# Kernel optimization log

Hardware: AMD Instinct MI355X
Metric: run time of the kernel (lower is better)

Reference implementation:

```python
import jax, jax.numpy as jnp
import numpy as np

NH = 4        # n_head
L_TOPK = 16   # AWG top-k l
DEC = 2       # dec_layers
EPS = 1e-6


def _ln(x, g, b):
    m = jnp.mean(x, -1, keepdims=True)
    v = jnp.mean((x - m) ** 2, -1, keepdims=True)
    return (x - m) * jax.lax.rsqrt(v + EPS) * g + b


def _heads(x, W):
    B, L, C = x.shape
    return (x @ W).reshape(B, L, NH, C // NH).transpose(0, 2, 1, 3)  # [B,H,L,dk]


def _softmax_attn(qh, kh):
    dk = qh.shape[-1]
    logits = jnp.einsum('bhqd,bhkd->bhqk', qh / jnp.sqrt(jnp.float32(dk)), kh)
    return jax.nn.softmax(logits, axis=-1)


def cross_attn_block(q, k, v, Wq, Wk, Wv, Wo, g, b):
    B, Lq, C = q.shape
    a = _softmax_attn(_heads(q, Wq), _heads(k, Wk))
    o = jnp.einsum('bhqk,bhkd->bhqd', a, _heads(v, Wv))
    o = o.transpose(0, 2, 1, 3).reshape(B, Lq, C) @ Wo
    return _ln(o + q, g, b)


def awg_attn_block(q, k, v, Wq, Wk, Wv, Wo, g, b):
    # top-k attention-weight-gating: keep weights >= l-th largest, renormalize
    B, Lq, C = q.shape
    a = _softmax_attn(_heads(q, Wq), _heads(k, Wk))
    thr = jax.lax.top_k(a, L_TOPK)[0][..., -1:]          # [B,H,Lq,1]
    w = a * (a >= thr).astype(a.dtype)
    w = w / jnp.sum(w, -1, keepdims=True)
    o = jnp.einsum('bhqk,bhkd->bhqd', w, _heads(v, Wv))
    o = o.transpose(0, 2, 1, 3).reshape(B, Lq, C) @ Wo
    return _ln(o + q, g, b)


def setup_inputs() -> dict:
    key = jax.random.key(0)
    ks = jax.random.split(key, 32)
    B, Lq, Lk, C, F = 4, 3000, 750, 64, 256
    s = 1.0 / np.sqrt(C)
    sf = 1.0 / np.sqrt(F)
    d = {}
    d['q'] = jax.random.normal(ks[0], (B, Lq, C), jnp.float32)
    d['enc'] = jax.random.normal(ks[1], (B, Lk, C), jnp.float32)
    # cross_attn_layer params
    for i, n in enumerate(['cal_Wq', 'cal_Wk', 'cal_Wv', 'cal_Wo']):
        d[n] = jax.random.normal(ks[2 + i], (C, C), jnp.float32) * s
    d['cal_ln1_g'] = jnp.ones((C,), jnp.float32)
    d['cal_ln1_b'] = jnp.zeros((C,), jnp.float32)
    d['cal_W1'] = jax.random.normal(ks[6], (C, F), jnp.float32) * s
    d['cal_b1'] = jnp.zeros((F,), jnp.float32)
    d['cal_W2'] = jax.random.normal(ks[7], (F, C), jnp.float32) * sf
    d['cal_b2'] = jnp.zeros((C,), jnp.float32)
    d['cal_ln2_g'] = jnp.ones((C,), jnp.float32)
    d['cal_ln2_b'] = jnp.zeros((C,), jnp.float32)
    # stacked MGAN params [DEC, ...]
    d['m_ln_g'] = jnp.ones((DEC, C), jnp.float32)
    d['m_ln_b'] = jnp.zeros((DEC, C), jnp.float32)
    d['m_fc1_W'] = jax.random.normal(ks[8], (DEC, C, C), jnp.float32) * s
    d['m_fc1_b'] = jnp.zeros((DEC, C), jnp.float32)
    d['m_fc2_W'] = jax.random.normal(ks[9], (DEC, C, C), jnp.float32) * s
    d['m_fc2_b'] = jnp.zeros((DEC, C), jnp.float32)
    for i, n in enumerate(['m_Wq', 'm_Wk', 'm_Wv', 'm_Wo']):
        d[n] = jax.random.normal(ks[10 + i], (DEC, C, C), jnp.float32) * s
    d['m_aln_g'] = jnp.ones((DEC, C), jnp.float32)
    d['m_aln_b'] = jnp.zeros((DEC, C), jnp.float32)
    d['fc_W'] = jax.random.normal(ks[14], (C, 1), jnp.float32) * s
    d['fc_b'] = jnp.zeros((1,), jnp.float32)
    return d


def reference(q, enc, cal_Wq, cal_Wk, cal_Wv, cal_Wo, cal_ln1_g, cal_ln1_b,
              cal_W1, cal_b1, cal_W2, cal_b2, cal_ln2_g, cal_ln2_b,
              m_ln_g, m_ln_b, m_fc1_W, m_fc1_b, m_fc2_W, m_fc2_b,
              m_Wq, m_Wk, m_Wv, m_Wo, m_aln_g, m_aln_b, fc_W, fc_b):
    # cross_attn_layer: attention + FFN + LN (dropout = identity in eval)
    x = cross_attn_block(q, enc, enc, cal_Wq, cal_Wk, cal_Wv, cal_Wo, cal_ln1_g, cal_ln1_b)
    ffn = jax.nn.relu(x @ cal_W1 + cal_b1) @ cal_W2 + cal_b2
    x = _ln(ffn + x, cal_ln2_g, cal_ln2_b)
    # MGAN decoder layers (rep_KV: k,v = encoder output)
    for i in range(DEC):
        qn = _ln(x, m_ln_g[i], m_ln_b[i])
        sg = jax.nn.sigmoid(qn @ m_fc1_W[i] + m_fc1_b[i]) * (qn @ m_fc2_W[i] + m_fc2_b[i])
        awg = awg_attn_block(sg, enc, enc, m_Wq[i], m_Wk[i], m_Wv[i], m_Wo[i],
                             m_aln_g[i], m_aln_b[i])
        # GLU(cat(sg, awg)) = sg * sigmoid(awg)
        x = qn + sg * jax.nn.sigmoid(awg)
    # label_type='p' head
    return jax.nn.sigmoid(x @ fc_W + fc_b)  # [B, Lq, 1]
```

## Files before the change

### kernel.cpp

```cpp
#include <hip/hip_runtime.h>
#include <hip/hip_bf16.h>

using bf16 = __hip_bfloat16;

#define DEV_INLINE __device__ __forceinline__

constexpr int B_  = 4;
constexpr int LQ  = 3000;
constexpr int LK  = 750;
constexpr int NH_ = 4;
constexpr float EPSF = 1e-6f;

constexpr int PITCH = 753;

constexpr size_t WS_KV = 0;
constexpr size_t WS_XB = 1152000;
constexpr size_t WS_QP = 1920000;
constexpr size_t WS_AO = 2688000;
constexpr size_t WS_QN = 3456000;
constexpr size_t WS_SG = 4224000;

typedef _Float16 half2_t __attribute__((ext_vector_type(2)));
typedef _Float16 half4_t __attribute__((ext_vector_type(4)));
typedef float    f32x4   __attribute__((ext_vector_type(4)));

#define MFMA16(a, b, c) __builtin_amdgcn_mfma_f32_16x16x16f16((a), (b), (c), 0, 0, 0)

DEV_INLINE float sigmoidf(float x) { return 1.f / (1.f + __expf(-x)); }

DEV_INLINE unsigned int packh2(float a, float b) {
  half2_t h = { (_Float16)a, (_Float16)b };
  unsigned int u; __builtin_memcpy(&u, &h, 4); return u;
}
DEV_INLINE half2_t u2h(unsigned int u) {
  half2_t h; __builtin_memcpy(&h, &u, 4); return h;
}
DEV_INLINE unsigned short f2h(float f) {
  _Float16 h = (_Float16)f;
  unsigned short u; __builtin_memcpy(&u, &h, 2); return u;
}
DEV_INLINE half4_t h4_from(const unsigned short* p) {
  unsigned int lo = *(const unsigned int*)p;
  unsigned int hi = *(const unsigned int*)(p + 2);
  unsigned long long v = ((unsigned long long)hi << 32) | lo;
  half4_t h; __builtin_memcpy(&h, &v, 8); return h;
}
DEV_INLINE float dot2(unsigned int kw, half2_t qh, float acc) {
  return __builtin_amdgcn_fdot2(u2h(kw), qh, acc, false);
}

DEV_INLINE unsigned int f2sort(float f) {
  int ib = __float_as_int(f);
  return (unsigned int)(ib ^ ((ib >> 31) | 0x80000000));
}

DEV_INLINE unsigned int bcastu(unsigned int v) {
  return (unsigned int)__builtin_amdgcn_readfirstlane((int)v);
}

DEV_INLINE float row_ln(float v, float g, float b) {
  float s1 = v, s2 = v * v;
  #pragma unroll
  for (int off = 32; off > 0; off >>= 1) {
    s1 += __shfl_xor(s1, off);
    s2 += __shfl_xor(s2, off);
  }
  const float m   = s1 * (1.f / 64.f);
  const float var = s2 * (1.f / 64.f) - m * m;
  return (v - m) * rsqrtf(var + EPSF) * g + b;
}

__global__ __launch_bounds__(256) void kvq_proj_kernel(
    const float* __restrict__ enc, const float* __restrict__ q,
    const float* __restrict__ calWq,
    const float* __restrict__ calWk, const float* __restrict__ calWv,
    const float* __restrict__ mWk, const float* __restrict__ mWv,
    float* __restrict__ kv, float* __restrict__ qp)
{
  const int y = blockIdx.y;
  if (y < 6 && blockIdx.x >= 188) return;
  __shared__ float Wl[64 * 65];
  __shared__ float xs[16][64];
  const int t = threadIdx.x, rr = t >> 6, cc = t & 63;
  const float* W;
  const float* src;
  float* dst;
  float scale = 1.f;
  int nrows = 3000;
  switch (y) {
    case 0: W = calWk; src = enc; dst = kv;               break;
    case 1: W = calWv; src = enc; dst = kv + 192000;      break;
    case 2: W = mWk;        src = enc; dst = kv + 384000; break;
    case 3: W = mWv;        src = enc; dst = kv + 576000; break;
    case 4: W = mWk + 4096; src = enc; dst = kv + 768000; break;
    case 5: W = mWv + 4096; src = enc; dst = kv + 960000; break;
    default: W = calWq; src = q; dst = qp; scale = 0.25f; nrows = 12000; break;
  }
  const bool packK = (y == 2) || (y == 4);
  for (int i = t; i < 4096; i += 256) Wl[(i >> 6) * 65 + (i & 63)] = W[i];
  const int base = blockIdx.x * 16;
  for (int i = t; i < 1024; i += 256) {
    const int grow = base + (i >> 6);
    xs[i >> 6][i & 63] = (grow < nrows) ? src[(size_t)grow * 64 + (i & 63)] : 0.f;
  }
  __syncthreads();
  #pragma unroll
  for (int p = 0; p < 4; ++p) {
    const int row = p * 4 + rr;
    const int grow = base + row;
    float acc = 0.f;
    #pragma unroll
    for (int c = 0; c < 64; ++c) acc = fmaf(xs[row][c], Wl[c * 65 + cc], acc);
    if (packK) {
      const float accN = __shfl_xor(acc, 1);
      if (!(cc & 1) && grow < nrows)
        ((unsigned int*)dst)[(size_t)grow * 32 + (cc >> 1)] = packh2(acc, accN);
    } else if (grow < nrows) {
      dst[(size_t)grow * 64 + cc] = acc * scale;
    }
  }
}

__global__ __launch_bounds__(256) void cross_attn_kernel(
    const float* __restrict__ qp, const float* __restrict__ kp,
    const float* __restrict__ vp, float* __restrict__ ao)
{
  extern __shared__ char smem[];
  unsigned short* Kl = (unsigned short*)smem;
  unsigned short* Vt = Kl + 750 * 18;
  unsigned short* Pt = Vt + 16 * 754;

  const int t = threadIdx.x;
  const int h = blockIdx.y, b = blockIdx.z;
  const float* kslab = kp + (size_t)(b * LK) * 64 + h * 16;
  const float* vslab = vp + (size_t)(b * LK) * 64 + h * 16;

  for (int k = t; k < LK; k += 256) {
    const float4* ks = (const float4*)(kslab + (size_t)k * 64);
    const float4* vs = (const float4*)(vslab + (size_t)k * 64);
    unsigned int* kr = (unsigned int*)(Kl + k * 18);
    #pragma unroll
    for (int q4 = 0; q4 < 4; ++q4) {
      float4 a = ks[q4], v = vs[q4];
      kr[q4 * 2]     = packh2(a.x, a.y);
      kr[q4 * 2 + 1] = packh2(a.z, a.w);
      Vt[(q4 * 4 + 0) * 754 + k] = f2h(v.x);
      Vt[(q4 * 4 + 1) * 754 + k] = f2h(v.y);
      Vt[(q4 * 4 + 2) * 754 + k] = f2h(v.z);
      Vt[(q4 * 4 + 3) * 754 + k] = f2h(v.w);
    }
  }
  if (t < 32) Vt[(t & 15) * 754 + 750 + (t >> 4)] = 0;
  __syncthreads();

  const int wave = t >> 6, lane = t & 63;
  const int col = lane & 15, quad = lane >> 4;
  const int qbase = blockIdx.x * 64 + wave * 16;
  unsigned short* Pt_w = Pt + wave * 288;

  int qrow = qbase + col; if (qrow >= LQ) qrow = LQ - 1;
  const float* qptr = qp + ((size_t)(b * LQ + qrow)) * 64 + h * 16 + quad * 4;
  half4_t aQ;
  {
    unsigned long long v = ((unsigned long long)packh2(qptr[2], qptr[3]) << 32)
                         | packh2(qptr[0], qptr[1]);
    __builtin_memcpy(&aQ, &v, 8);
  }

  f32x4 O = {0.f, 0.f, 0.f, 0.f};
  float Zp[4] = {0.f, 0.f, 0.f, 0.f};
  const f32x4 zeroC = {0.f, 0.f, 0.f, 0.f};

  for (int tile = 0; tile < 47; ++tile) {
    const int key = tile * 16 + col;
    const half4_t bK = h4_from(Kl + key * 18 + quad * 4);
    f32x4 S = MFMA16(aQ, bK, zeroC);
    const bool valid = key < LK;
    float e0 = valid ? __expf(S[0]) : 0.f;
    float e1 = valid ? __expf(S[1]) : 0.f;
    float e2 = valid ? __expf(S[2]) : 0.f;
    float e3 = valid ? __expf(S[3]) : 0.f;
    Zp[0] += e0; Zp[1] += e1; Zp[2] += e2; Zp[3] += e3;
    Pt_w[(quad * 4 + 0) * 18 + col] = f2h(e0);
    Pt_w[(quad * 4 + 1) * 18 + col] = f2h(e1);
    Pt_w[(quad * 4 + 2) * 18 + col] = f2h(e2);
    Pt_w[(quad * 4 + 3) * 18 + col] = f2h(e3);
    const half4_t aP = h4_from(Pt_w + col * 18 + quad * 4);
    const half4_t bV = h4_from(Vt + col * 754 + tile * 16 + quad * 4);
    O = MFMA16(aP, bV, O);
  }

  #pragma unroll
  for (int r = 0; r < 4; ++r) {
    float z = Zp[r];
    z += __shfl_xor(z, 1);
    z += __shfl_xor(z, 2);
    z += __shfl_xor(z, 4);
    z += __shfl_xor(z, 8);
    Zp[r] = z;
  }

  #pragma unroll
  for (int r = 0; r < 4; ++r) {
    const int orow = qbase + quad * 4 + r;
    if (orow < LQ)
      ao[((size_t)(b * LQ + orow)) * 64 + h * 16 + col] = O[r] / Zp[r];
  }
}

__global__ __launch_bounds__(512) void awg_attn_kernel(
    const float* __restrict__ qp, const unsigned int* __restrict__ kp,
    const float* __restrict__ vp, float* __restrict__ ao)
{
  extern __shared__ char smem[];
  uint2*          KT2   = (uint2*)smem;
  unsigned short* candi = (unsigned short*)(smem + 4 * PITCH * 8);
  float*          cw    = (float*)(smem + 4 * PITCH * 8 + 2048);
  unsigned short* ciw   = (unsigned short*)(smem + 4 * PITCH * 8 + 2048 + 1536);

  const int t = threadIdx.x;
  const int h = blockIdx.y, b = blockIdx.z;
  const unsigned int* kslab = kp + ((size_t)(b * LK)) * 32 + h * 8;

  for (int k = t; k < LK; k += 512) {
    const uint2* ks = (const uint2*)(kslab + (size_t)k * 32);
    #pragma unroll
    for (int d4 = 0; d4 < 4; ++d4) KT2[d4 * PITCH + k] = ks[d4];
  }
  __syncthreads();

  const int wave = t >> 6, lane = t & 63;
  const unsigned long long below = (1ull << lane) - 1ull;
  unsigned short* ci0 = candi + wave * 128;
  unsigned short* ci1 = ci0 + 64;
  float* cw0 = cw + wave * 48;      float* cw1 = cw0 + 24;
  unsigned short* cio0 = ciw + wave * 48; unsigned short* cio1 = cio0 + 24;

  const int r0 = blockIdx.x * 16 + wave * 2;
  int r0r = r0; if (r0r > LQ - 2) r0r = LQ - 2;
  const float* qrow = qp + ((size_t)(b * LQ + r0r)) * 64 + h * 16;
  unsigned int qw0[8], qw1[8];
  #pragma unroll
  for (int i = 0; i < 8; ++i) {
    qw0[i] = bcastu(packh2(qrow[2 * i], qrow[2 * i + 1]));
    qw1[i] = bcastu(packh2(qrow[64 + 2 * i], qrow[64 + 2 * i + 1]));
  }

  float lg0[12], lg1[12];
  #pragma unroll
  for (int tt = 0; tt < 12; ++tt) {
    const int k = lane + (tt << 6);
    if (tt < 11 || k < LK) {
      float a0 = 0.f, a1 = 0.f;
      #pragma unroll
      for (int d4 = 0; d4 < 4; ++d4) {
        const uint2 w = KT2[d4 * PITCH + k];
        a0 = dot2(w.x, u2h(qw0[2 * d4]), a0); a0 = dot2(w.y, u2h(qw0[2 * d4 + 1]), a0);
        a1 = dot2(w.x, u2h(qw1[2 * d4]), a1); a1 = dot2(w.y, u2h(qw1[2 * d4 + 1]), a1);
      }
      lg0[tt] = a0; lg1[tt] = a1;
    } else {
      lg0[tt] = -3.0e38f; lg1[tt] = -3.0e38f;
    }
  }

  float fm0 = lg0[0], fm1 = lg1[0];
  #pragma unroll
  for (int tt = 1; tt < 12; ++tt) { fm0 = fmaxf(fm0, lg0[tt]); fm1 = fmaxf(fm1, lg1[tt]); }
  float M0 = fm0, M1 = fm1;
  #pragma unroll
  for (int off = 32; off > 0; off >>= 1) {
    M0 = fmaxf(M0, __shfl_xor(M0, off));
    M1 = fmaxf(M1, __shfl_xor(M1, off));
  }
  const unsigned int head0 = f2sort(fm0), head1 = f2sort(fm1);

  unsigned int L0 = 0u, L1 = 0u;
  #pragma unroll
  for (int bit = 31; bit >= 20; --bit) {
    const unsigned int c0 = L0 | (1u << bit);
    const unsigned int c1 = L1 | (1u << bit);
    if (__popcll(__ballot(head0 >= c0)) >= 16) L0 = c0;
    if (__popcll(__ballot(head1 >= c1)) >= 16) L1 = c1;
  }

  int base0 = 0, base1 = 0;
  #pragma unroll
  for (int tt = 0; tt < 12; ++tt) {
    const int k = lane + (tt << 6);
    const bool p0 = f2sort(lg0[tt]) >= L0;
    const bool p1 = f2sort(lg1[tt]) >= L1;
    const unsigned long long m0 = __ballot(p0);
    const unsigned long long m1 = __ballot(p1);
    if (p0) {
      const int pos = base0 + __popcll(m0 & below);
      if (pos < 64) ci0[pos] = (unsigned short)k;
    }
    if (p1) {
      const int pos = base1 + __popcll(m1 & below);
      if (pos < 64) ci1[pos] = (unsigned short)k;
    }
    base0 += __popcll(m0);
    base1 += __popcll(m1);
  }
  const int C0 = min(base0, 64), C1 = min(base1, 64);

  const int k0 = (lane < C0) ? (int)ci0[lane] : 0;
  const int k1 = (lane < C1) ? (int)ci1[lane] : 0;
  float cv0 = 0.f, cv1 = 0.f;
  #pragma unroll
  for (int d4 = 0; d4 < 4; ++d4) {
    const uint2 wa = KT2[d4 * PITCH + k0];
    const uint2 wb = KT2[d4 * PITCH + k1];
    cv0 = dot2(wa.x, u2h(qw0[2 * d4]), cv0); cv0 = dot2(wa.y, u2h(qw0[2 * d4 + 1]), cv0);
    cv1 = dot2(wb.x, u2h(qw1[2 * d4]), cv1); cv1 = dot2(wb.y, u2h(qw1[2 * d4 + 1]), cv1);
  }
  const unsigned int cu0 = (lane < C0) ? f2sort(cv0) : 0u;
  const unsigned int cu1 = (lane < C1) ? f2sort(cv1) : 0u;

  unsigned int T0 = 0u, T1 = 0u;
  #pragma unroll
  for (int bit = 31; bit >= 0; --bit) {
    const unsigned int c0 = T0 | (1u << bit);
    const unsigned int c1 = T1 | (1u << bit);
    if (__popcll(__ballot(cu0 >= c0)) >= 16) T0 = c0;
    if (__popcll(__ballot(cu1 >= c1)) >= 16) T1 = c1;
  }

  const bool w0 = (lane < C0) && (cu0 >= T0);
  const bool w1 = (lane < C1) && (cu1 >= T1);
  const unsigned long long mw0 = __ballot(w0);
  const unsigned long long mw1 = __ballot(w1);
  const int cnt0 = min((int)__popcll(mw0), 24);
  const int cnt1 = min((int)__popcll(mw1), 24);
  if (w0) {
    const int pos = __popcll(mw0 & below);
    if (pos < 24) { cw0[pos] = cv0; cio0[pos] = (unsigned short)k0; }
  }
  if (w1) {
    const int pos = __popcll(mw1 & below);
    if (pos < 24) { cw1[pos] = cv1; cio1[pos] = (unsigned short)k1; }
  }

  const int dd = lane & 15;
  const int rsel = (lane >> 4) & 1;
  const int half = lane >> 5;
  const int cnt = rsel ? cnt1 : cnt0;
  const float* cwr = rsel ? cw1 : cw0;
  const unsigned short* cir = rsel ? cio1 : cio0;
  const float ref = rsel ? M1 : M0;
  const float* vbase = vp + (size_t)(b * LK) * 64 + h * 16 + dd;
  float acc = 0.f, Z = 0.f;
  for (int j = half; j < cnt; j += 2) {
    const float e = __expf(cwr[j] - ref);
    Z += e;
    acc = fmaf(e, vbase[(size_t)cir[j] * 64], acc);
  }
  acc += __shfl_xor(acc, 32);
  Z   += __shfl_xor(Z, 32);
  if (lane < 32 && (r0 + rsel) < LQ)
    ao[((size_t)(b * LQ + r0 + rsel)) * 64 + h * 16 + dd] = acc / Z;
}

__global__ __launch_bounds__(256) void cross_ffn_kernel(
    const float* __restrict__ ao, const float* __restrict__ qres,
    const float* __restrict__ Wo,
    const float* __restrict__ g1, const float* __restrict__ b1n,
    const float* __restrict__ W1, const float* __restrict__ bb1,
    const float* __restrict__ W2, const float* __restrict__ bb2,
    const float* __restrict__ g2, const float* __restrict__ b2n,
    float* __restrict__ xout)
{
  __shared__ float xs[8][64];
  __shared__ float hs[8][256];
  const int t = threadIdx.x, rr = t >> 6, cc = t & 63;
  const size_t base = (size_t)blockIdx.x * 8;
  for (int i = t; i < 512; i += 256) xs[i >> 6][i & 63] = ao[base * 64 + i];
  __syncthreads();
  float acc[2];
  #pragma unroll
  for (int p = 0; p < 2; ++p) {
    const int row = p * 4 + rr;
    float a = 0.f;
    #pragma unroll
    for (int c = 0; c < 64; ++c) a = fmaf(xs[row][c], Wo[c * 64 + cc], a);
    acc[p] = a + qres[(base + row) * 64 + cc];
  }
  __syncthreads();
  #pragma unroll
  for (int p = 0; p < 2; ++p) {
    const int row = p * 4 + rr;
    xs[row][cc] = row_ln(acc[p], g1[cc], b1n[cc]);
  }
  __syncthreads();
  {
    float hv[8];
    #pragma unroll
    for (int r = 0; r < 8; ++r) hv[r] = 0.f;
    #pragma unroll 8
    for (int c = 0; c < 64; ++c) {
      const float w = W1[c * 256 + t];
      #pragma unroll
      for (int r = 0; r < 8; ++r) hv[r] = fmaf(xs[r][c], w, hv[r]);
    }
    const float bb = bb1[t];
    #pragma unroll
    for (int r = 0; r < 8; ++r) hs[r][t] = fmaxf(hv[r] + bb, 0.f);
  }
  __syncthreads();
  float acc2[2];
  #pragma unroll
  for (int p = 0; p < 2; ++p) acc2[p] = bb2[cc];
  #pragma unroll 8
  for (int c = 0; c < 256; ++c) {
    const float w = W2[c * 64 + cc];
    acc2[0] = fmaf(hs[rr][c], w, acc2[0]);
    acc2[1] = fmaf(hs[4 + rr][c], w, acc2[1]);
  }
  #pragma unroll
  for (int p = 0; p < 2; ++p) {
    const int row = p * 4 + rr;
    const float a = acc2[p] + xs[row][cc];
    xout[(base + row) * 64 + cc] = row_ln(a, g2[cc], b2n[cc]);
  }
}

__global__ __launch_bounds__(256) void mgan_pre_kernel(
    const float* __restrict__ x, const float* __restrict__ lng,
    const float* __restrict__ lnb, const float* __restrict__ W1,
    const float* __restrict__ bb1, const float* __restrict__ W2,
    const float* __restrict__ bb2, const float* __restrict__ Wq,
    float* __restrict__ qn, float* __restrict__ sg, float* __restrict__ qp)
{
  __shared__ float qs[8][64];
  __shared__ float sgs[8][64];
  const int t = threadIdx.x, rr = t >> 6, cc = t & 63;
  const size_t base = (size_t)blockIdx.x * 8;
  #pragma unroll
  for (int p = 0; p < 2; ++p) {
    const int row = p * 4 + rr;
    const float v = x[(base + row) * 64 + cc];
    const float qv = row_ln(v, lng[cc], lnb[cc]);
    qn[(base + row) * 64 + cc] = qv;
    qs[row][cc] = qv;
  }
  __syncthreads();
  float d1[2], d2[2];
  #pragma unroll
  for (int p = 0; p < 2; ++p) { d1[p] = bb1[cc]; d2[p] = bb2[cc]; }
  #pragma unroll 4
  for (int c = 0; c < 64; ++c) {
    const float w1 = W1[c * 64 + cc];
    const float w2 = W2[c * 64 + cc];
    #pragma unroll
    for (int p = 0; p < 2; ++p) {
      const float xv = qs[p * 4 + rr][c];
      d1[p] = fmaf(xv, w1, d1[p]);
      d2[p] = fmaf(xv, w2, d2[p]);
    }
  }
  #pragma unroll
  for (int p = 0; p < 2; ++p) {
    const int row = p * 4 + rr;
    const float sv = sigmoidf(d1[p]) * d2[p];
    sg[(base + row) * 64 + cc] = sv;
    sgs[row][cc] = sv;
  }
  __syncthreads();
  #pragma unroll
  for (int p = 0; p < 2; ++p) {
    const int row = p * 4 + rr;
    float a = 0.f;
    #pragma unroll
    for (int c = 0; c < 64; ++c) a = fmaf(sgs[row][c], Wq[c * 64 + cc], a);
    qp[(base + row) * 64 + cc] = a * 0.25f;
  }
}

__global__ __launch_bounds__(256) void out_pre_kernel(
    const float* __restrict__ ao, const float* __restrict__ sg,
    const float* __restrict__ qn, const float* __restrict__ Wo,
    const float* __restrict__ g_, const float* __restrict__ b_,
    const float* __restrict__ lng, const float* __restrict__ lnb,
    const float* __restrict__ W1, const float* __restrict__ bb1,
    const float* __restrict__ W2, const float* __restrict__ bb2,
    const float* __restrict__ Wq,
    float* __restrict__ qn_out, float* __restrict__ sg_out,
    float* __restrict__ qp_out)
{
  __shared__ float xs[8][64];
  __shared__ float sgs[8][64];
  const int t = threadIdx.x, rr = t >> 6, cc = t & 63;
  const size_t base = (size_t)blockIdx.x * 8;
  for (int i = t; i < 512; i += 256) xs[i >> 6][i & 63] = ao[base * 64 + i];
  __syncthreads();
  float accp[2], sgv[2];
  #pragma unroll
  for (int p = 0; p < 2; ++p) {
    const int row = p * 4 + rr;
    const size_t idx = (base + row) * 64 + cc;
    float a = 0.f;
    #pragma unroll
    for (int c = 0; c < 64; ++c) a = fmaf(xs[row][c], Wo[c * 64 + cc], a);
    sgv[p] = sg[idx];
    accp[p] = a + sgv[p];
  }
  __syncthreads();
  #pragma unroll
  for (int p = 0; p < 2; ++p) {
    const int row = p * 4 + rr;
    const size_t idx = (base + row) * 64 + cc;
    const float awg = row_ln(accp[p], g_[cc], b_[cc]);
    const float xv = qn[idx] + sgv[p] * sigmoidf(awg);
    const float qv = row_ln(xv, lng[cc], lnb[cc]);
    qn_out[idx] = qv;
    xs[row][cc] = qv;
  }
  __syncthreads();
  float d1[2], d2[2];
  #pragma unroll
  for (int p = 0; p < 2; ++p) { d1[p] = bb1[cc]; d2[p] = bb2[cc]; }
  #pragma unroll 4
  for (int c = 0; c < 64; ++c) {
    const float w1 = W1[c * 64 + cc];
    const float w2 = W2[c * 64 + cc];
    #pragma unroll
    for (int p = 0; p < 2; ++p) {
      const float xv = xs[p * 4 + rr][c];
      d1[p] = fmaf(xv, w1, d1[p]);
      d2[p] = fmaf(xv, w2, d2[p]);
    }
  }
  __syncthreads();
  #pragma unroll
  for (int p = 0; p < 2; ++p) {
    const int row = p * 4 + rr;
    const size_t idx = (base + row) * 64 + cc;
    const float sv = sigmoidf(d1[p]) * d2[p];
    sg_out[idx] = sv;
    sgs[row][cc] = sv;
  }
  __syncthreads();
  #pragma unroll
  for (int p = 0; p < 2; ++p) {
    const int row = p * 4 + rr;
    float a = 0.f;
    #pragma unroll
    for (int c = 0; c < 64; ++c) a = fmaf(sgs[row][c], Wq[c * 64 + cc], a);
    qp_out[(base + row) * 64 + cc] = a * 0.25f;
  }
}

__global__ __launch_bounds__(256) void out_final_kernel(
    const float* __restrict__ ao, const float* __restrict__ sg,
    const float* __restrict__ qn, const float* __restrict__ Wo,
    const float* __restrict__ g_, const float* __restrict__ b_,
    const float* __restrict__ fw, const float* __restrict__ fb,
    float* __restrict__ out)
{
  __shared__ float xs[8][64];
  const int t = threadIdx.x, rr = t >> 6, cc = t & 63;
  const size_t base = (size_t)blockIdx.x * 8;
  for (int i = t; i < 512; i += 256) xs[i >> 6][i & 63] = ao[base * 64 + i];
  __syncthreads();
  #pragma unroll
  for (int p = 0; p < 2; ++p) {
    const int row = p * 4 + rr;
    const size_t idx = (base + row) * 64 + cc;
    float a = 0.f;
    #pragma unroll
    for (int c = 0; c < 64; ++c) a = fmaf(xs[row][c], Wo[c * 64 + cc], a);
    const float sgv = sg[idx];
    a += sgv;
    const float awg = row_ln(a, g_[cc], b_[cc]);
    const float xv = qn[idx] + sgv * sigmoidf(awg);
    float v = xv * fw[cc];
    #pragma unroll
    for (int off = 32; off > 0; off >>= 1) v += __shfl_xor(v, off);
    if (cc == 0) out[base + row] = sigmoidf(v + fb[0]);
  }
}

extern "C" void kernel_launch(void* const* d_in, const int* in_sizes, int n_in,
                              void* d_out, int out_size, void* d_ws, size_t ws_size,
                              hipStream_t stream) {
  (void)in_sizes; (void)n_in; (void)out_size; (void)ws_size;

  const float* q     = (const float*)d_in[0];
  const float* enc   = (const float*)d_in[1];
  const float* calWq = (const float*)d_in[2];
  const float* calWk = (const float*)d_in[3];
  const float* calWv = (const float*)d_in[4];
  const float* calWo = (const float*)d_in[5];
  const float* ln1g  = (const float*)d_in[6];
  const float* ln1b  = (const float*)d_in[7];
  const float* W1    = (const float*)d_in[8];
  const float* b1v   = (const float*)d_in[9];
  const float* W2    = (const float*)d_in[10];
  const float* b2v   = (const float*)d_in[11];
  const float* ln2g  = (const float*)d_in[12];
  const float* ln2b  = (const float*)d_in[13];
  const float* mlng  = (const float*)d_in[14];
  const float* mlnb  = (const float*)d_in[15];
  const float* mfc1W = (const float*)d_in[16];
  const float* mfc1b = (const float*)d_in[17];
  const float* mfc2W = (const float*)d_in[18];
  const float* mfc2b = (const float*)d_in[19];
  const float* mWq   = (const float*)d_in[20];
  const float* mWk   = (const float*)d_in[21];
  const float* mWv   = (const float*)d_in[22];
  const float* mWo   = (const float*)d_in[23];
  const float* malng = (const float*)d_in[24];
  const float* malnb = (const float*)d_in[25];
  const float* fcW   = (const float*)d_in[26];
  const float* fcb   = (const float*)d_in[27];
  float* out = (float*)d_out;

  float* ws  = (float*)d_ws;
  float* kv  = ws + WS_KV;
  float* qp  = ws + WS_QP;
  float* aob = ws + WS_AO;
  float* qnb = ws + WS_QN;
  float* sgb = ws + WS_SG;
  float* xb  = ws + WS_XB;

  const size_t crossLds = (750 * 18 + 16 * 754 + 4 * 288) * 2;
  const size_t awgLds   = 4 * PITCH * 8 + 2048 + 1536 + 768;

  kvq_proj_kernel<<<dim3(750, 7), 256, 0, stream>>>(enc, q, calWq, calWk, calWv,
                                                    mWk, mWv, kv, qp);

  cross_attn_kernel<<<dim3(47, NH_, B_), 256, crossLds, stream>>>(qp, kv, kv + 192000, aob);
  cross_ffn_kernel<<<1500, 256, 0, stream>>>(aob, q, calWo, ln1g, ln1b,
                                             W1, b1v, W2, b2v, ln2g, ln2b, xb);

  mgan_pre_kernel<<<1500, 256, 0, stream>>>(xb, mlng, mlnb, mfc1W, mfc1b,
                                            mfc2W, mfc2b, mWq, qnb, sgb, qp);
  awg_attn_kernel<<<dim3(188, NH_, B_), 512, awgLds, stream>>>(
      qp, (const unsigned int*)(kv + 2 * 192000), kv + 3 * 192000, aob);
  out_pre_kernel<<<1500, 256, 0, stream>>>(aob, sgb, qnb, mWo, malng, malnb,
                                           mlng + 64, mlnb + 64,
                                           mfc1W + 4096, mfc1b + 64,
                                           mfc2W + 4096, mfc2b + 64,
                                           mWq + 4096, qnb, sgb, qp);

  awg_attn_kernel<<<dim3(188, NH_, B_), 512, awgLds, stream>>>(
      qp, (const unsigned int*)(kv + 4 * 192000), kv + 5 * 192000, aob);
  out_final_kernel<<<1500, 256, 0, stream>>>(aob, sgb, qnb, mWo + 4096,
                                             malng + 64, malnb + 64, fcW, fcb, out);
}
```

Before: 361.1 us.

## Process four query rows per wave in AWG attention with radix-4 top-k search

Each wave in the AWG attention kernel now handles four query rows instead of two, so every K value read from LDS is reused across four dot products, and the grid is halved. Candidate logits are stored alongside their indices, so the second QK recompute is dropped. The bitwise threshold searches resolve two bits per step using three ballots. The value gather is restructured so each 16-lane group handles one row over a fixed 24 slots padded with sentinels. This costs more registers (4x12 logits), so occupancy may drop, and fewer blocks are launched.

```diff
diff --git a/kernel.cpp b/kernel.cpp
--- a/kernel.cpp
+++ b/kernel.cpp
@@ -214,9 +214,10 @@
 {
   extern __shared__ char smem[];
   uint2*          KT2   = (uint2*)smem;
-  unsigned short* candi = (unsigned short*)(smem + 4 * PITCH * 8);
-  float*          cw    = (float*)(smem + 4 * PITCH * 8 + 2048);
-  unsigned short* ciw   = (unsigned short*)(smem + 4 * PITCH * 8 + 2048 + 1536);
+  unsigned short* candK = (unsigned short*)(smem + 4 * PITCH * 8);
+  float*          candV = (float*)(smem + 4 * PITCH * 8 + 4096);
+  float*          selW  = (float*)(smem + 4 * PITCH * 8 + 4096 + 8192);
+  unsigned short* selK  = (unsigned short*)(smem + 4 * PITCH * 8 + 4096 + 8192 + 3072);
 
   const int t = threadIdx.x;
   const int h = blockIdx.y, b = blockIdx.z;
@@ -231,134 +232,149 @@
 
   const int wave = t >> 6, lane = t & 63;
   const unsigned long long below = (1ull << lane) - 1ull;
-  unsigned short* ci0 = candi + wave * 128;
-  unsigned short* ci1 = ci0 + 64;
-  float* cw0 = cw + wave * 48;      float* cw1 = cw0 + 24;
-  unsigned short* cio0 = ciw + wave * 48; unsigned short* cio1 = cio0 + 24;
-
-  const int r0 = blockIdx.x * 16 + wave * 2;
-  int r0r = r0; if (r0r > LQ - 2) r0r = LQ - 2;
+  unsigned short* cK = candK + wave * 256;
+  float*          cV = candV + wave * 256;
+  float*          sW = selW + wave * 96;
+  unsigned short* sK = selK + wave * 96;
+
+  sW[lane] = -3.0e38f; sK[lane] = 0;
+  if (lane < 32) { sW[64 + lane] = -3.0e38f; sK[64 + lane] = 0; }
+
+  const int r0 = blockIdx.x * 32 + wave * 4;
+  int r0r = r0; if (r0r > LQ - 4) r0r = LQ - 4;
   const float* qrow = qp + ((size_t)(b * LQ + r0r)) * 64 + h * 16;
-  unsigned int qw0[8], qw1[8];
-  #pragma unroll
-  for (int i = 0; i < 8; ++i) {
-    qw0[i] = bcastu(packh2(qrow[2 * i], qrow[2 * i + 1]));
-    qw1[i] = bcastu(packh2(qrow[64 + 2 * i], qrow[64 + 2 * i + 1]));
-  }
-
-  float lg0[12], lg1[12];
+  unsigned int qw[4][8];
+  #pragma unroll
+  for (int r = 0; r < 4; ++r) {
+    #pragma unroll
+    for (int i = 0; i < 8; ++i)
+      qw[r][i] = bcastu(packh2(qrow[r * 64 + 2 * i], qrow[r * 64 + 2 * i + 1]));
+  }
+
+  float lg[4][12];
   #pragma unroll
   for (int tt = 0; tt < 12; ++tt) {
     const int k = lane + (tt << 6);
     if (tt < 11 || k < LK) {
-      float a0 = 0.f, a1 = 0.f;
+      float a0 = 0.f, a1 = 0.f, a2 = 0.f, a3 = 0.f;
       #pragma unroll
       for (int d4 = 0; d4 < 4; ++d4) {
         const uint2 w = KT2[d4 * PITCH + k];
-        a0 = dot2(w.x, u2h(qw0[2 * d4]), a0); a0 = dot2(w.y, u2h(qw0[2 * d4 + 1]), a0);
-        a1 = dot2(w.x, u2h(qw1[2 * d4]), a1); a1 = dot2(w.y, u2h(qw1[2 * d4 + 1]), a1);
+        a0 = dot2(w.x, u2h(qw[0][2 * d4]), a0); a0 = dot2(w.y, u2h(qw[0][2 * d4 + 1]), a0);
+        a1 = dot2(w.x, u2h(qw[1][2 * d4]), a1); a1 = dot2(w.y, u2h(qw[1][2 * d4 + 1]), a1);
+        a2 = dot2(w.x, u2h(qw[2][2 * d4]), a2); a2 = dot2(w.y, u2h(qw[2][2 * d4 + 1]), a2);
+        a3 = dot2(w.x, u2h(qw[3][2 * d4]), a3); a3 = dot2(w.y, u2h(qw[3][2 * d4 + 1]), a3);
       }
-      lg0[tt] = a0; lg1[tt] = a1;
+      lg[0][tt] = a0; lg[1][tt] = a1; lg[2][tt] = a2; lg[3][tt] = a3;
     } else {
-      lg0[tt] = -3.0e38f; lg1[tt] = -3.0e38f;
-    }
-  }
-
-  float fm0 = lg0[0], fm1 = lg1[0];
-  #pragma unroll
-  for (int tt = 1; tt < 12; ++tt) { fm0 = fmaxf(fm0, lg0[tt]); fm1 = fmaxf(fm1, lg1[tt]); }
-  float M0 = fm0, M1 = fm1;
-  #pragma unroll
-  for (int off = 32; off > 0; off >>= 1) {
-    M0 = fmaxf(M0, __shfl_xor(M0, off));
-    M1 = fmaxf(M1, __shfl_xor(M1, off));
-  }
-  const unsigned int head0 = f2sort(fm0), head1 = f2sort(fm1);
-
-  unsigned int L0 = 0u, L1 = 0u;
-  #pragma unroll
-  for (int bit = 31; bit >= 20; --bit) {
-    const unsigned int c0 = L0 | (1u << bit);
-    const unsigned int c1 = L1 | (1u << bit);
-    if (__popcll(__ballot(head0 >= c0)) >= 16) L0 = c0;
-    if (__popcll(__ballot(head1 >= c1)) >= 16) L1 = c1;
-  }
-
-  int base0 = 0, base1 = 0;
+      lg[0][tt] = -3.0e38f; lg[1][tt] = -3.0e38f;
+      lg[2][tt] = -3.0e38f; lg[3][tt] = -3.0e38f;
+    }
+  }
+
+  float fm[4], M[4];
+  #pragma unroll
+  for (int r = 0; r < 4; ++r) {
+    float m = lg[r][0];
+    #pragma unroll
+    for (int tt = 1; tt < 12; ++tt) m = fmaxf(m, lg[r][tt]);
+    fm[r] = m;
+  }
+  #pragma unroll
+  for (int r = 0; r < 4; ++r) {
+    float m = fm[r];
+    #pragma unroll
+    for (int off = 32; off > 0; off >>= 1) m = fmaxf(m, __shfl_xor(m, off));
+    M[r] = m;
+  }
+
+  unsigned int hsort[4];
+  #pragma unroll
+  for (int r = 0; r < 4; ++r) hsort[r] = f2sort(fm[r]);
+  unsigned int L[4] = {0u, 0u, 0u, 0u};
+  #pragma unroll
+  for (int bpos = 30; bpos >= 20; bpos -= 2) {
+    #pragma unroll
+    for (int r = 0; r < 4; ++r) {
+      const unsigned int c3 = L[r] | (3u << bpos);
+      const unsigned int c2 = L[r] | (2u << bpos);
+      const unsigned int c1 = L[r] | (1u << bpos);
+      const int n3 = (int)__popcll(__ballot(hsort[r] >= c3));
+      const int n2 = (int)__popcll(__ballot(hsort[r] >= c2));
+      const int n1 = (int)__popcll(__ballot(hsort[r] >= c1));
+      L[r] |= (n3 >= 16) ? (3u << bpos) : (n2 >= 16) ? (2u << bpos)
+            : (n1 >= 16) ? (1u << bpos) : 0u;
+    }
+  }
+
+  int cb[4] = {0, 0, 0, 0};
   #pragma unroll
   for (int tt = 0; tt < 12; ++tt) {
     const int k = lane + (tt << 6);
-    const bool p0 = f2sort(lg0[tt]) >= L0;
-    const bool p1 = f2sort(lg1[tt]) >= L1;
-    const unsigned long long m0 = __ballot(p0);
-    const unsigned long long m1 = __ballot(p1);
-    if (p0) {
-      const int pos = base0 + __popcll(m0 & below);
-      if (pos < 64) ci0[pos] = (unsigned short)k;
-    }
-    if (p1) {
-      const int pos = base1 + __popcll(m1 & below);
-      if (pos < 64) ci1[pos] = (unsigned short)k;
-    }
-    base0 += __popcll(m0);
-    base1 += __popcll(m1);
-  }
-  const int C0 = min(base0, 64), C1 = min(base1, 64);
-
-  const int k0 = (lane < C0) ? (int)ci0[lane] : 0;
-  const int k1 = (lane < C1) ? (int)ci1[lane] : 0;
-  float cv0 = 0.f, cv1 = 0.f;
-  #pragma unroll
-  for (int d4 = 0; d4 < 4; ++d4) {
-    const uint2 wa = KT2[d4 * PITCH + k0];
-    const uint2 wb = KT2[d4 * PITCH + k1];
-    cv0 = dot2(wa.x, u2h(qw0[2 * d4]), cv0); cv0 = dot2(wa.y, u2h(qw0[2 * d4 + 1]), cv0);
-    cv1 = dot2(wb.x, u2h(qw1[2 * d4]), cv1); cv1 = dot2(wb.y, u2h(qw1[2 * d4 + 1]), cv1);
-  }
-  const unsigned int cu0 = (lane < C0) ? f2sort(cv0) : 0u;
-  const unsigned int cu1 = (lane < C1) ? f2sort(cv1) : 0u;
-
-  unsigned int T0 = 0u, T1 = 0u;
-  #pragma unroll
-  for (int bit = 31; bit >= 0; --bit) {
-    const unsigned int c0 = T0 | (1u << bit);
-    const unsigned int c1 = T1 | (1u << bit);
-    if (__popcll(__ballot(cu0 >= c0)) >= 16) T0 = c0;
-    if (__popcll(__ballot(cu1 >= c1)) >= 16) T1 = c1;
-  }
-
-  const bool w0 = (lane < C0) && (cu0 >= T0);
-  const bool w1 = (lane < C1) && (cu1 >= T1);
-  const unsigned long long mw0 = __ballot(w0);
-  const unsigned long long mw1 = __ballot(w1);
-  const int cnt0 = min((int)__popcll(mw0), 24);
-  const int cnt1 = min((int)__popcll(mw1), 24);
-  if (w0) {
-    const int pos = __popcll(mw0 & below);
-    if (pos < 24) { cw0[pos] = cv0; cio0[pos] = (unsigned short)k0; }
-  }
-  if (w1) {
-    const int pos = __popcll(mw1 & below);
-    if (pos < 24) { cw1[pos] = cv1; cio1[pos] = (unsigned short)k1; }
+    #pragma unroll
+    for (int r = 0; r < 4; ++r) {
+      const bool p = f2sort(lg[r][tt]) >= L[r];
+      const unsigned long long m = __ballot(p);
+      if (p) {
+        const int pos = cb[r] + (int)__popcll(m & below);
+        if (pos < 64) { cK[r * 64 + pos] = (unsigned short)k; cV[r * 64 + pos] = lg[r][tt]; }
+      }
+      cb[r] += (int)__popcll(m);
+    }
+  }
+  int C[4];
+  #pragma unroll
+  for (int r = 0; r < 4; ++r) C[r] = min(cb[r], 64);
+
+  unsigned int cu[4]; float cv[4]; int ck[4];
+  #pragma unroll
+  for (int r = 0; r < 4; ++r) {
+    const bool has = lane < C[r];
+    cv[r] = has ? cV[r * 64 + lane] : 0.f;
+    ck[r] = has ? (int)cK[r * 64 + lane] : 0;
+    cu[r] = has ? f2sort(cv[r]) : 0u;
+  }
+
+  unsigned int T[4] = {0u, 0u, 0u, 0u};
+  #pragma unroll
+  for (int bpos = 30; bpos >= 0; bpos -= 2) {
+    #pragma unroll
+    for (int r = 0; r < 4; ++r) {
+      const unsigned int c3 = T[r] | (3u << bpos);
+      const unsigned int c2 = T[r] | (2u << bpos);
+      const unsigned int c1 = T[r] | (1u << bpos);
+      const int n3 = (int)__popcll(__ballot(cu[r] >= c3));
+      const int n2 = (int)__popcll(__ballot(cu[r] >= c2));
+      const int n1 = (int)__popcll(__ballot(cu[r] >= c1));
+      T[r] |= (n3 >= 16) ? (3u << bpos) : (n2 >= 16) ? (2u << bpos)
+            : (n1 >= 16) ? (1u << bpos) : 0u;
+    }
+  }
+
+  #pragma unroll
+  for (int r = 0; r < 4; ++r) {
+    const bool w = (lane < C[r]) && (cu[r] >= T[r]);
+    const unsigned long long mw = __ballot(w);
+    if (w) {
+      const int pos = (int)__popcll(mw & below);
+      if (pos < 24) { sW[r * 24 + pos] = cv[r]; sK[r * 24 + pos] = (unsigned short)ck[r]; }
+    }
   }
 
   const int dd = lane & 15;
-  const int rsel = (lane >> 4) & 1;
-  const int half = lane >> 5;
-  const int cnt = rsel ? cnt1 : cnt0;
-  const float* cwr = rsel ? cw1 : cw0;
-  const unsigned short* cir = rsel ? cio1 : cio0;
-  const float ref = rsel ? M1 : M0;
+  const int rsel = lane >> 4;
+  const float ref = (rsel == 0) ? M[0] : (rsel == 1) ? M[1] : (rsel == 2) ? M[2] : M[3];
+  const float* cwr = sW + rsel * 24;
+  const unsigned short* cir = sK + rsel * 24;
   const float* vbase = vp + (size_t)(b * LK) * 64 + h * 16 + dd;
   float acc = 0.f, Z = 0.f;
-  for (int j = half; j < cnt; j += 2) {
+  #pragma unroll
+  for (int j = 0; j < 24; ++j) {
     const float e = __expf(cwr[j] - ref);
     Z += e;
     acc = fmaf(e, vbase[(size_t)cir[j] * 64], acc);
   }
-  acc += __shfl_xor(acc, 32);
-  Z   += __shfl_xor(Z, 32);
-  if (lane < 32 && (r0 + rsel) < LQ)
+  if (r0 + rsel < LQ)
     ao[((size_t)(b * LQ + r0 + rsel)) * 64 + h * 16 + dd] = acc / Z;
 }
 
@@ -625,7 +641,7 @@
   float* xb  = ws + WS_XB;
 
   const size_t crossLds = (750 * 18 + 16 * 754 + 4 * 288) * 2;
-  const size_t awgLds   = 4 * PITCH * 8 + 2048 + 1536 + 768;
+  const size_t awgLds   = 4 * PITCH * 8 + 4096 + 8192 + 3072 + 1536;
 
   kvq_proj_kernel<<<dim3(750, 7), 256, 0, stream>>>(enc, q, calWq, calWk, calWv,
                                                     mWk, mWv, kv, qp);
@@ -636,7 +652,7 @@
 
   mgan_pre_kernel<<<1500, 256, 0, stream>>>(xb, mlng, mlnb, mfc1W, mfc1b,
                                             mfc2W, mfc2b, mWq, qnb, sgb, qp);
-  awg_attn_kernel<<<dim3(188, NH_, B_), 512, awgLds, stream>>>(
+  awg_attn_kernel<<<dim3(94, NH_, B_), 512, awgLds, stream>>>(
       qp, (const unsigned int*)(kv + 2 * 192000), kv + 3 * 192000, aob);
   out_pre_kernel<<<1500, 256, 0, stream>>>(aob, sgb, qnb, mWo, malng, malnb,
                                            mlng + 64, mlnb + 64,
@@ -644,7 +660,7 @@
                                            mfc2W + 4096, mfc2b + 64,
                                            mWq + 4096, qnb, sgb, qp);
 
-  awg_attn_kernel<<<dim3(188, NH_, B_), 512, awgLds, stream>>>(
+  awg_attn_kernel<<<dim3(94, NH_, B_), 512, awgLds, stream>>>(
       qp, (const unsigned int*)(kv + 4 * 192000), kv + 5 * 192000, aob);
   out_final_kernel<<<1500, 256, 0, stream>>>(aob, sgb, qnb, mWo + 4096,
                                              malng + 64, malnb + 64, fcW, fcb, out);
```

After: 369.1 us. +2.2%, slower.
